# Kernel tuning notes

Hardware: AMD Instinct MI355X
Metric: run time of the kernel (lower is better)

Reference implementation:

```python
import jax, jax.numpy as jnp
import numpy as np

D_MODEL = 1024
N_HEADS = 16
D_K = D_MODEL // N_HEADS


def setup_inputs() -> dict:
    key = jax.random.key(0)
    ks = jax.random.split(key, 7)
    B, S, D = 2, 2048, D_MODEL
    scale = 1.0 / np.sqrt(D)
    return {
        "query": jax.random.normal(ks[0], (B, S, D), dtype=jnp.float32),
        "key": jax.random.normal(ks[1], (B, S, D), dtype=jnp.float32),
        "value": jax.random.normal(ks[2], (B, S, D), dtype=jnp.float32),
        "w_q": jax.random.normal(ks[3], (D, D), dtype=jnp.float32) * scale,
        "w_k": jax.random.normal(ks[4], (D, D), dtype=jnp.float32) * scale,
        "w_v": jax.random.normal(ks[5], (D, D), dtype=jnp.float32) * scale,
        "w_o": jax.random.normal(ks[6], (D, D), dtype=jnp.float32) * scale,
    }


def reference(query, key, value, w_q, w_k, w_v, w_o):
    B, S, D = query.shape
    H, Dk = N_HEADS, D_K
    # nn.Linear (no bias): x @ W.T ; then split heads -> [B, H, S, Dk]
    def split_heads(x, W):
        return (x @ W.T).reshape(B, S, H, Dk).transpose(0, 2, 1, 3)
    Q = split_heads(query, w_q)
    K = split_heads(key, w_k)
    V = split_heads(value, w_v)
    scores = jnp.einsum("bhqd,bhkd->bhqk", Q, K) / np.sqrt(Dk).astype(jnp.float32)
    attn = jax.nn.softmax(scores, axis=-1)  # dropout is identity in eval
    attended = jnp.einsum("bhqk,bhkd->bhqd", attn, V)
    attended = attended.transpose(0, 2, 1, 3).reshape(B, S, D)
    output = attended @ w_o.T
    avg_attention = attn.mean(axis=1)  # mean over heads -> [B, S, S]
    return (output, avg_attention)
```

## Files before the change

### kernel.cpp

```cpp
#include <hip/hip_runtime.h>
#include <math.h>

#define SEQ 2048
#define DMODEL 1024
#define NH 16
#define DK 64
#define BATCH 2

using bf16x8 = __attribute__((ext_vector_type(8))) __bf16;
using bf16x4 = __attribute__((ext_vector_type(4))) __bf16;
using f32x4  = __attribute__((ext_vector_type(4))) float;

__device__ inline f32x4 mfma16(bf16x8 a, bf16x8 b, f32x4 c) {
    return __builtin_amdgcn_mfma_f32_16x16x32_bf16(a, b, c, 0, 0, 0);
}

__device__ inline void load_lds16(const void* g, void* l) {
    __builtin_amdgcn_global_load_lds(
        (const __attribute__((address_space(1))) void*)g,
        (__attribute__((address_space(3))) void*)l, 16, 0, 0);
}

#define EXP_SCALE 0.18033688011112042f

__global__ __launch_bounds__(256) void conv_bf16(
        const float* __restrict__ q, const float* __restrict__ k,
        const float* __restrict__ v, const float* __restrict__ wq,
        const float* __restrict__ wk, const float* __restrict__ wv,
        const float* __restrict__ wo,
        __bf16* __restrict__ oq, __bf16* __restrict__ ok, __bf16* __restrict__ ov,
        __bf16* __restrict__ owq, __bf16* __restrict__ owk,
        __bf16* __restrict__ owv, __bf16* __restrict__ owo) {
    int bid = blockIdx.x;
    const float* src;
    __bf16* dst;
    size_t off;
    if (bid < 3072) {
        int ti = bid >> 10;
        src = ti == 0 ? q : (ti == 1 ? k : v);
        dst = ti == 0 ? oq : (ti == 1 ? ok : ov);
        off = (size_t)(bid & 1023) * 4096;
    } else {
        int ti = (bid - 3072) >> 8;
        src = ti == 0 ? wq : (ti == 1 ? wk : (ti == 2 ? wv : wo));
        dst = ti == 0 ? owq : (ti == 1 ? owk : (ti == 2 ? owv : owo));
        off = (size_t)((bid - 3072) & 255) * 4096;
    }
    src += off; dst += off;
    const int t = threadIdx.x;
#pragma unroll
    for (int i = 0; i < 4; ++i) {
        float4 x = *(const float4*)(src + t * 4 + i * 1024);
        bf16x4 y;
        y[0] = (__bf16)x.x; y[1] = (__bf16)x.y;
        y[2] = (__bf16)x.z; y[3] = (__bf16)x.w;
        *(bf16x4*)(dst + t * 4 + i * 1024) = y;
    }
}

__device__ __forceinline__ void gemm_core(const __bf16* __restrict__ A,
                                          const __bf16* __restrict__ B,
                                          void* __restrict__ out, int mode,
                                          int m0, int n0, int N,
                                          __bf16* As, __bf16* Bs) {
    const int t    = threadIdx.x;
    const int w    = t >> 6;
    const int lane = t & 63;
    const int m    = lane & 15;
    const int kg   = lane >> 4;
    const int wr   = w >> 1, wc = w & 1;

    auto stage = [&](int buf, int k0) {
#pragma unroll
        for (int i = 0; i < 4; ++i) {
            const int ablk = w * 4 + i;
            const int mt = ablk >> 1, kt = ablk & 1;
            const __bf16* ga = A + (size_t)(m0 + mt * 16 + m) * 1024 + k0 + kt * 32 + kg * 8;
            load_lds16(ga, &As[buf * 8192 + ablk * 512]);
        }
#pragma unroll
        for (int i = 0; i < 2; ++i) {
            const int bblk = w * 2 + i;
            const int nt = bblk >> 1, kt = bblk & 1;
            const __bf16* gb = B + (size_t)(n0 + nt * 16 + m) * 1024 + k0 + kt * 32 + kg * 8;
            load_lds16(gb, &Bs[buf * 4096 + bblk * 512]);
        }
    };

    f32x4 acc[4][2] = {};

    stage(0, 0);
    __syncthreads();

    int cur = 0;
    for (int k0 = 0; k0 < 1024; k0 += 64) {
        if (k0 + 64 < 1024) stage(cur ^ 1, k0 + 64);
        const __bf16* Ac = &As[cur * 8192];
        const __bf16* Bc = &Bs[cur * 4096];
#pragma unroll
        for (int kt = 0; kt < 2; ++kt) {
            bf16x8 af[4], bg[2];
#pragma unroll
            for (int i = 0; i < 4; ++i)
                af[i] = *(const bf16x8*)&Ac[((wr * 4 + i) * 2 + kt) * 512 + lane * 8];
#pragma unroll
            for (int j = 0; j < 2; ++j)
                bg[j] = *(const bf16x8*)&Bc[((wc * 2 + j) * 2 + kt) * 512 + lane * 8];
#pragma unroll
            for (int i = 0; i < 4; ++i)
#pragma unroll
                for (int j = 0; j < 2; ++j)
                    acc[i][j] = mfma16(af[i], bg[j], acc[i][j]);
        }
        __syncthreads();
        cur ^= 1;
    }

#pragma unroll
    for (int i = 0; i < 4; ++i) {
        const int rb = m0 + wr * 64 + i * 16 + kg * 4;
#pragma unroll
        for (int j = 0; j < 2; ++j) {
            const int gc = n0 + wc * 32 + j * 16 + m;
#pragma unroll
            for (int r = 0; r < 4; ++r) {
                const int gr = rb + r;
                const float vv = acc[i][j][r];
                if (mode == 0) {
                    ((float*)out)[(size_t)gr * N + gc] = vv;
                } else if (mode == 1) {
                    ((__bf16*)out)[(size_t)gr * N + gc] = (__bf16)vv;
                } else {
                    const int hh = gr >> 6, dd = gr & 63;
                    const int bb = gc >> 11, ss = gc & 2047;
                    ((__bf16*)out)[(((size_t)bb * NH + hh) * DK + dd) * SEQ + ss] = (__bf16)vv;
                }
            }
        }
    }
}

__device__ __forceinline__ int xcd_swz(int s, int cpx) {
    return (s & 7) * cpx + (s >> 3);
}

__global__ __launch_bounds__(256) void gemm_qkv(
        const __bf16* __restrict__ Xq, const __bf16* __restrict__ Wq, __bf16* Qr,
        const __bf16* __restrict__ Xk, const __bf16* __restrict__ Wk, __bf16* Kr,
        const __bf16* __restrict__ Xv, const __bf16* __restrict__ Wv, __bf16* Vt) {
    __shared__ __align__(16) __bf16 As[16384];
    __shared__ __align__(16) __bf16 Bs[8192];
    const int bid = blockIdx.x;
    if (bid < 512) {
        const int s = xcd_swz(bid, 64);
        gemm_core(Xq, Wq, Qr, 1, (s >> 4) * 128, (s & 15) * 64, 1024, As, Bs);
    } else if (bid < 1024) {
        const int s = xcd_swz(bid - 512, 64);
        gemm_core(Xk, Wk, Kr, 1, (s >> 4) * 128, (s & 15) * 64, 1024, As, Bs);
    } else {
        const int s = xcd_swz(bid - 1024, 64);
        gemm_core(Wv, Xv, Vt, 2, (s >> 6) * 128, (s & 63) * 64, 4096, As, Bs);
    }
}

__global__ __launch_bounds__(512) void attn_flash(const __bf16* __restrict__ Qr,
                                                  const __bf16* __restrict__ Kr,
                                                  const __bf16* __restrict__ Vt,
                                                  __bf16* __restrict__ att,
                                                  float* __restrict__ invs) {
    __shared__ __align__(16) unsigned char smem[49664];
    __bf16* KbA  = (__bf16*)smem;
    __bf16* VbA  = KbA + 8192;
    __bf16* PbA  = VbA + 8192;
    float*  sinv = (float*)(smem + 49152);

    const int t    = threadIdx.x;
    const int w    = t >> 6;
    const int lane = t & 63;
    const int m    = lane & 15;
    const int kg   = lane >> 4;

    const int L  = xcd_swz(blockIdx.x, 64);
    const int b  = L >> 8;
    const int h  = (L >> 4) & 15;
    const int qw = (L & 15) * 128 + w * 16;

    const __bf16* Kh = Kr + (size_t)b * SEQ * 1024 + h * 64;
    const __bf16* Vh = Vt + ((size_t)b * NH + h) * DK * SEQ;
    __bf16* Pw = PbA + w * 1024;

    const size_t rowQ = (size_t)(b * SEQ + qw + m) * 1024 + h * 64 + kg * 8;
    const bf16x8 qa = *(const bf16x8*)(Qr + rowQ);
    const bf16x8 qb = *(const bf16x8*)(Qr + rowQ + 32);

    const int srow = t >> 3;
    const int su   = t & 7;
    const int sus  = (su ^ (srow & 7)) * 8;
    auto stage = [&](int buf, int kt) {
        load_lds16(Kh + (size_t)(kt + srow) * 1024 + sus, KbA + buf * 4096 + w * 512);
        load_lds16(Vh + (size_t)srow * SEQ + kt + sus,    VbA + buf * 4096 + w * 512);
    };

    f32x4 pv[4] = {};
    float rsum = 0.f;

    stage(0, 0);
    __syncthreads();

    int cur = 0;
    for (int kt = 0; kt < SEQ; kt += 64) {
        if (kt + 64 < SEQ) stage(cur ^ 1, kt + 64);
        const __bf16* Kc = KbA + cur * 4096;
        const __bf16* Vc = VbA + cur * 4096;
#pragma unroll
        for (int nt = 0; nt < 4; ++nt) {
            const int row = nt * 16 + m;
            bf16x8 k0 = *(const bf16x8*)&Kc[row * 64 + ((kg ^ (m & 7)) * 8)];
            bf16x8 k1 = *(const bf16x8*)&Kc[row * 64 + (((kg + 4) ^ (m & 7)) * 8)];
            f32x4 c = {};
            c = mfma16(k0, qa, c);
            c = mfma16(k1, qb, c);
            bf16x4 pk;
#pragma unroll
            for (int r = 0; r < 4; ++r) {
                float p = exp2f(c[r] * EXP_SCALE);
                rsum += p;
                pk[r] = (__bf16)p;
            }
            const int off8  = nt * 4 + kg;
            const int off8s = (((off8 >> 1) ^ (m & 7)) << 1) | (off8 & 1);
            *(bf16x4*)&Pw[m * 64 + off8s * 4] = pk;
        }
#pragma unroll
        for (int ks = 0; ks < 2; ++ks) {
            const int u = (ks * 4 + kg) ^ (m & 7);
            bf16x8 pa = *(const bf16x8*)&Pw[m * 64 + u * 8];
#pragma unroll
            for (int nt = 0; nt < 4; ++nt) {
                bf16x8 vb = *(const bf16x8*)&Vc[(nt * 16 + m) * 64 + u * 8];
                pv[nt] = mfma16(pa, vb, pv[nt]);
            }
        }
        __syncthreads();
        cur ^= 1;
    }

    rsum += __shfl_xor(rsum, 16);
    rsum += __shfl_xor(rsum, 32);
    const float inv = 1.0f / rsum;
    if (lane < 16) {
        sinv[w * 16 + m] = inv;
        invs[((size_t)b * NH + h) * SEQ + qw + m] = inv;
    }
    __syncthreads();
    float iv[4];
#pragma unroll
    for (int r = 0; r < 4; ++r) iv[r] = sinv[w * 16 + kg * 4 + r];

    float* scf = (float*)smem + w * 1088;
#pragma unroll
    for (int nt = 0; nt < 4; ++nt)
#pragma unroll
        for (int r = 0; r < 4; ++r)
            scf[(kg * 4 + r) * 68 + nt * 16 + m] = pv[nt][r] * iv[r];
    __syncthreads();
    {
        const int q = lane >> 2, c0 = (lane & 3) * 16;
        const float* srcf = &scf[q * 68 + c0];
        bf16x8 o0, o1;
#pragma unroll
        for (int j = 0; j < 8; ++j) {
            o0[j] = (__bf16)srcf[j];
            o1[j] = (__bf16)srcf[j + 8];
        }
        __bf16* dst = att + (size_t)(b * SEQ + qw + q) * DMODEL + h * DK + c0;
        *(bf16x8*)(dst)     = o0;
        *(bf16x8*)(dst + 8) = o1;
    }
}

__device__ __forceinline__ void avg_core(const __bf16* __restrict__ Qr,
                                         const __bf16* __restrict__ Kr,
                                         const float* __restrict__ invs,
                                         float* __restrict__ avg,
                                         int L, __bf16* Kb) {
    const int t    = threadIdx.x;
    const int w    = t >> 6;
    const int lane = t & 63;
    const int m    = lane & 15;
    const int kg   = lane >> 4;
    const int b    = L >> 9;
    const int s0   = ((L >> 5) & 15) * 128;
    const int qw   = (L & 31) * 64 + w * 16;

    const __bf16* Kbase = Kr + (size_t)(b * SEQ + s0) * 1024;

    auto stageK = [&](int buf, int h) {
#pragma unroll
        for (int s = 0; s < 4; ++s) {
            const int i   = w * 4 + s;
            const int row = i * 8 + (lane >> 3);
            const int u   = lane & 7;
            load_lds16(Kbase + (size_t)row * 1024 + h * 64 + ((u ^ (row & 7)) * 8),
                       Kb + buf * 8192 + i * 512);
        }
    };

    f32x4 acc[8] = {};

    stageK(0, 0);
    const size_t qoff = (size_t)(b * SEQ + qw + m) * 1024 + kg * 8;
    bf16x8 a0 = *(const bf16x8*)(Qr + qoff);
    bf16x8 a1 = *(const bf16x8*)(Qr + qoff + 32);
    f32x4 ivr = *(const f32x4*)&invs[(size_t)b * NH * SEQ + qw + kg * 4];
    __syncthreads();

    int cur = 0;
    for (int h = 0; h < NH; ++h) {
        if (h + 1 < NH) stageK(cur ^ 1, h + 1);
        bf16x8 na0, na1;
        f32x4 nivr;
        if (h + 1 < NH) {
            na0  = *(const bf16x8*)(Qr + qoff + (h + 1) * 64);
            na1  = *(const bf16x8*)(Qr + qoff + (h + 1) * 64 + 32);
            nivr = *(const f32x4*)&invs[((size_t)b * NH + h + 1) * SEQ + qw + kg * 4];
        }
        const __bf16* Kc = Kb + cur * 8192;
#pragma unroll
        for (int nt = 0; nt < 8; ++nt) {
            const int row = nt * 16 + m;
            bf16x8 k0 = *(const bf16x8*)&Kc[row * 64 + ((kg ^ (m & 7)) * 8)];
            bf16x8 k1 = *(const bf16x8*)&Kc[row * 64 + (((kg + 4) ^ (m & 7)) * 8)];
            f32x4 c = {};
            c = mfma16(a0, k0, c);
            c = mfma16(a1, k1, c);
#pragma unroll
            for (int r = 0; r < 4; ++r)
                acc[nt][r] += ivr[r] * exp2f(c[r] * EXP_SCALE);
        }
        __syncthreads();
        cur ^= 1;
        a0 = na0; a1 = na1; ivr = nivr;
    }

    const float sc = 1.0f / NH;
#pragma unroll
    for (int nt = 0; nt < 8; ++nt)
#pragma unroll
        for (int r = 0; r < 4; ++r)
            avg[(size_t)(b * SEQ + qw + kg * 4 + r) * SEQ + s0 + nt * 16 + m] =
                acc[nt][r] * sc;
}

__global__ __launch_bounds__(256) void gemm_wo_avg(
        const __bf16* __restrict__ At, const __bf16* __restrict__ Wo,
        float* __restrict__ out,
        const __bf16* __restrict__ Qr, const __bf16* __restrict__ Kr,
        const float* __restrict__ invs, float* __restrict__ avg) {
    __shared__ __align__(16) __bf16 sm[24576];
    const int bid = blockIdx.x;
    if (bid < 512) {
        const int s = xcd_swz(bid, 64);
        gemm_core(At, Wo, out, 0, (s >> 4) * 128, (s & 15) * 64, 1024,
                  sm, sm + 16384);
    } else {
        avg_core(Qr, Kr, invs, avg, xcd_swz(bid - 512, 128), sm);
    }
}

extern "C" void kernel_launch(void* const* d_in, const int* in_sizes, int n_in,
                              void* d_out, int out_size, void* d_ws, size_t ws_size,
                              hipStream_t stream) {
    const float* query = (const float*)d_in[0];
    const float* key   = (const float*)d_in[1];
    const float* value = (const float*)d_in[2];
    const float* w_q   = (const float*)d_in[3];
    const float* w_k   = (const float*)d_in[4];
    const float* w_v   = (const float*)d_in[5];
    const float* w_o   = (const float*)d_in[6];

    float* out = (float*)d_out;
    float* avg = out + (size_t)BATCH * SEQ * DMODEL;

    __bf16* Xq = (__bf16*)d_ws;
    __bf16* Xk = Xq + 4194304;
    __bf16* Xv = Xk + 4194304;
    __bf16* Wq = Xv + 4194304;
    __bf16* Wk = Wq + 1048576;
    __bf16* Wv = Wk + 1048576;
    __bf16* Wo = Wv + 1048576;
    __bf16* Qr = Wo + 1048576;
    __bf16* Kr = Qr + 4194304;
    __bf16* Vt = Kr + 4194304;
    float*  Invs = (float*)(Vt + 4194304);
    __bf16* At = Xq;

    conv_bf16<<<4096, 256, 0, stream>>>(query, key, value, w_q, w_k, w_v, w_o,
                                        Xq, Xk, Xv, Wq, Wk, Wv, Wo);

    gemm_qkv<<<1536, 256, 0, stream>>>(Xq, Wq, Qr, Xk, Wk, Kr, Xv, Wv, Vt);

    attn_flash<<<512, 512, 0, stream>>>(Qr, Kr, Vt, At, Invs);

    gemm_wo_avg<<<1536, 256, 0, stream>>>(At, Wo, out, Qr, Kr, Invs, avg);
}
```

Before: 305.9 us.

## Prefetch two stages ahead with explicit vmcnt waits instead of syncthreads

```diff
diff --git a/kernel.cpp b/kernel.cpp
--- a/kernel.cpp
+++ b/kernel.cpp
@@ -20,6 +20,9 @@
         (const __attribute__((address_space(1))) void*)g,
         (__attribute__((address_space(3))) void*)l, 16, 0, 0);
 }
+
+#define VMCNT(n) asm volatile("s_waitcnt vmcnt(" #n ")" ::: "memory")
+#define BARRIER() __builtin_amdgcn_s_barrier()
 
 #define EXP_SCALE 0.18033688011112042f
 
@@ -90,11 +93,12 @@
     f32x4 acc[4][2] = {};
 
     stage(0, 0);
-    __syncthreads();
+    stage(1, 64);
+    VMCNT(6);
+    BARRIER();
 
     int cur = 0;
     for (int k0 = 0; k0 < 1024; k0 += 64) {
-        if (k0 + 64 < 1024) stage(cur ^ 1, k0 + 64);
         const __bf16* Ac = &As[cur * 8192];
         const __bf16* Bc = &Bs[cur * 4096];
 #pragma unroll
@@ -112,7 +116,14 @@
                 for (int j = 0; j < 2; ++j)
                     acc[i][j] = mfma16(af[i], bg[j], acc[i][j]);
         }
-        __syncthreads();
+        BARRIER();
+        if (k0 + 128 < 1024) {
+            stage(cur, k0 + 128);
+            VMCNT(6);
+        } else {
+            VMCNT(0);
+        }
+        BARRIER();
         cur ^= 1;
     }
 
@@ -205,11 +216,12 @@
     float rsum = 0.f;
 
     stage(0, 0);
-    __syncthreads();
+    stage(1, 64);
+    VMCNT(2);
+    BARRIER();
 
     int cur = 0;
     for (int kt = 0; kt < SEQ; kt += 64) {
-        if (kt + 64 < SEQ) stage(cur ^ 1, kt + 64);
         const __bf16* Kc = KbA + cur * 4096;
         const __bf16* Vc = VbA + cur * 4096;
 #pragma unroll
@@ -241,7 +253,14 @@
                 pv[nt] = mfma16(pa, vb, pv[nt]);
             }
         }
-        __syncthreads();
+        BARRIER();
+        if (kt + 128 < SEQ) {
+            stage(cur, kt + 128);
+            VMCNT(2);
+        } else {
+            VMCNT(0);
+        }
+        BARRIER();
         cur ^= 1;
     }
 
@@ -308,16 +327,18 @@
 
     f32x4 acc[8] = {};
 
-    stageK(0, 0);
     const size_t qoff = (size_t)(b * SEQ + qw + m) * 1024 + kg * 8;
     bf16x8 a0 = *(const bf16x8*)(Qr + qoff);
     bf16x8 a1 = *(const bf16x8*)(Qr + qoff + 32);
     f32x4 ivr = *(const f32x4*)&invs[(size_t)b * NH * SEQ + qw + kg * 4];
-    __syncthreads();
+
+    stageK(0, 0);
+    stageK(1, 1);
+    VMCNT(4);
+    BARRIER();
 
     int cur = 0;
     for (int h = 0; h < NH; ++h) {
-        if (h + 1 < NH) stageK(cur ^ 1, h + 1);
         bf16x8 na0, na1;
         f32x4 nivr;
         if (h + 1 < NH) {
@@ -338,7 +359,14 @@
             for (int r = 0; r < 4; ++r)
                 acc[nt][r] += ivr[r] * exp2f(c[r] * EXP_SCALE);
         }
-        __syncthreads();
+        BARRIER();
+        if (h + 2 < NH) {
+            stageK(cur, h + 2);
+            VMCNT(4);
+        } else {
+            VMCNT(0);
+        }
+        BARRIER();
         cur ^= 1;
         a0 = na0; a1 = na1; ivr = nivr;
     }
```

After: 314.3 us. 1.03x slower.
